# Performance work log

Measured on AMD Instinct MI355X. Metric: run time of the kernel, lower is better.

The kernel has to match this reference:

```python
import jax, jax.numpy as jnp
import numpy as np
from jax import lax

B_, L_ = 2, 512
D_MODEL, EXPAND, HEAD_DIM, NGROUPS, D_STATE, D_CONV = 512, 2, 64, 1, 64, 3
D_INNER = EXPAND * D_MODEL            # 1024
NHEADS = D_INNER // HEAD_DIM          # 16
CONV_DIM = D_INNER + 2 * NGROUPS * D_STATE   # 1152
D_IN_PROJ = 2 * D_INNER + 2 * NGROUPS * D_STATE + NHEADS  # 2192
RMS_EPS = 1e-5


def silu(x):
    return x * jax.nn.sigmoid(x)


def segsum(x):
    # x: (..., T) -> (..., T, T); out[..., i, j] = sum_{j<k<=i} x[..., k], -inf above diag
    T = x.shape[-1]
    xr = jnp.broadcast_to(x[..., None], x.shape + (T,))
    keep = jnp.tril(jnp.ones((T, T), dtype=bool), -1)
    xr = jnp.where(keep, xr, 0.0)
    s = jnp.cumsum(xr, axis=-2)
    diag = jnp.tril(jnp.ones((T, T), dtype=bool), 0)
    return jnp.where(diag, s, -jnp.inf)


def ssd(x, A, Bm, Cm, chunk):
    # x: (b,l,h,p), A: (b,l,h), Bm/Cm: (b,l,g,n); chunk==1 as in the source forward
    b, l, h, p = x.shape
    c = l // chunk
    n = Bm.shape[-1]
    x = x.reshape(b, c, chunk, h, p)
    Bm = Bm.reshape(b, c, chunk, Bm.shape[2], n)
    Cm = Cm.reshape(b, c, chunk, Cm.shape[2], n)
    A = A.reshape(b, c, chunk, h).transpose(0, 3, 1, 2)        # (b,h,c,l)
    A_cumsum = jnp.cumsum(A, axis=-1)
    Lmat = jnp.exp(segsum(A))                                   # (b,h,c,l,l)
    # broadcast group dim (g==1) to heads, matching torch.einsum broadcasting
    Bb = jnp.broadcast_to(Bm, (b, c, chunk, h, n))
    Cb = jnp.broadcast_to(Cm, (b, c, chunk, h, n))
    Y_diag = jnp.einsum('bclhn,bcshn,bhcls,bcshp->bclhp', Cb, Bb, Lmat, x)
    decay_states = jnp.exp(A_cumsum[:, :, :, -1:] - A_cumsum)   # (b,h,c,l)
    states = jnp.einsum('bclhn,bhcl,bclhp->bchpn', Bb, decay_states, x)
    states = jnp.concatenate([jnp.zeros_like(states[:, :1]), states], axis=1)  # (b,c+1,h,p,n)
    A_last = jnp.pad(A_cumsum[:, :, :, -1], ((0, 0), (0, 0), (1, 0)))          # (b,h,c+1)
    decay_chunk = jnp.exp(segsum(A_last))                       # (b,h,c+1,c+1)
    new_states = jnp.einsum('bhzc,bchpn->bzhpn', decay_chunk, states)
    states = new_states[:, :-1]                                 # (b,c,h,p,n)
    state_decay_out = jnp.exp(A_cumsum)
    Y_off = jnp.einsum('bclhn,bchpn,bhcl->bclhp', Cb, states, state_decay_out)
    return (Y_diag + Y_off).reshape(b, l, h, p)


def causal_dwconv(x, w, bias):
    # x: (B,L,C); w: (C,K) depthwise; torch pads (K-1) both sides then slices [:L] == left-pad only
    xt = x.transpose(0, 2, 1)
    y = lax.conv_general_dilated(xt, w[:, None, :], (1,), [(D_CONV - 1, 0)],
                                 feature_group_count=CONV_DIM,
                                 dimension_numbers=('NCH', 'OIH', 'NCH'))
    return y.transpose(0, 2, 1) + bias


def setup_inputs() -> dict:
    key = jax.random.key(0)
    ks = jax.random.split(key, 8)
    u = jax.random.normal(ks[0], (B_, L_, D_MODEL), dtype=jnp.float32)
    W_in = jax.random.normal(ks[1], (D_MODEL, D_IN_PROJ), dtype=jnp.float32) / np.sqrt(D_MODEL).astype(np.float32)
    conv_w = jax.random.normal(ks[2], (CONV_DIM, D_CONV), dtype=jnp.float32) * 0.3
    conv_b = jnp.zeros((CONV_DIM,), dtype=jnp.float32)
    dt = jnp.exp(jax.random.uniform(ks[3], (NHEADS,), dtype=jnp.float32)
                 * (np.float32(np.log(0.1)) - np.float32(np.log(0.001))) + np.float32(np.log(0.001)))
    dt = jnp.clip(dt, 1e-4, None)
    dt_bias = dt + jnp.log(-jnp.expm1(-dt))
    A_log = jnp.log(jax.random.uniform(ks[4], (NHEADS,), dtype=jnp.float32, minval=1.0, maxval=16.0))
    D_param = jnp.ones((NHEADS,), dtype=jnp.float32)
    rms_w = jnp.ones((D_INNER,), dtype=jnp.float32)
    W_out = jax.random.normal(ks[5], (D_INNER, D_MODEL), dtype=jnp.float32) / np.sqrt(D_INNER).astype(np.float32)
    return {"u": u, "W_in": W_in, "conv_w": conv_w, "conv_b": conv_b, "dt_bias": dt_bias,
            "A_log": A_log, "D_param": D_param, "rms_w": rms_w, "W_out": W_out}


def reference(u, W_in, conv_w, conv_b, dt_bias, A_log, D_param, rms_w, W_out):
    b, l, _ = u.shape
    zxbcdt = u @ W_in                                   # (b,l,D_IN_PROJ)
    z = zxbcdt[..., :D_INNER]
    xBC = zxbcdt[..., D_INNER:D_INNER + CONV_DIM]
    dt = zxbcdt[..., D_INNER + CONV_DIM:]
    dt = jax.nn.softplus(dt + dt_bias)                  # (b,l,h)
    A = -jnp.exp(A_log)                                 # (h,)
    xBC = silu(causal_dwconv(xBC, conv_w, conv_b))      # (b,l,CONV_DIM)
    x = xBC[..., :D_INNER].reshape(b, l, NHEADS, HEAD_DIM)
    Bm = xBC[..., D_INNER:D_INNER + D_STATE][:, :, None, :]     # (b,l,1,n)
    Cm = xBC[..., D_INNER + D_STATE:][:, :, None, :]            # (b,l,1,n)
    y = ssd(x * dt[..., None], A * dt, Bm, Cm, 1)       # (b,l,h,p)
    y = y + x * D_param[:, None]
    y = y.reshape(b, l, D_INNER)
    # gated RMSNorm
    yz = y * silu(z)
    y = yz * lax.rsqrt(jnp.mean(yz * yz, axis=-1, keepdims=True) + RMS_EPS) * rms_w
    return y @ W_out
```

## Files before the change

### kernel.cpp

```cpp
#include <hip/hip_runtime.h>
#include <hip/hip_bf16.h>

#define B_SZ 2
#define L_SZ 512
#define D_MODEL 512
#define D_INNER 1024
#define HEAD_DIM 64
#define NHEADS 16
#define D_STATE 64
#define D_CONV 3
#define CONV_DIM 1152
#define D_IN_PROJ 2192
#define BL (B_SZ * L_SZ)
#define RMS_EPS 1e-5f
#define QC 64
#define NCH 8
#define NPAD1 2304
#define PB 72

typedef __attribute__((ext_vector_type(8))) short short8t;
typedef __attribute__((ext_vector_type(8))) unsigned short ushort8t;
typedef __attribute__((ext_vector_type(4))) unsigned short ushort4t;
typedef __attribute__((ext_vector_type(4))) float f32x4;

__device__ __forceinline__ unsigned short f2bf(float f) {
    unsigned u = __float_as_uint(f);
    u += 0x7fff + ((u >> 16) & 1);
    return (unsigned short)(u >> 16);
}
__device__ __forceinline__ float bf2f(unsigned short u) {
    return __uint_as_float(((unsigned)u) << 16);
}

__device__ __forceinline__ void gload_lds16(const void* g, void* lds) {
    __builtin_amdgcn_global_load_lds(
        (const __attribute__((address_space(1))) unsigned int*)g,
        (__attribute__((address_space(3))) unsigned int*)lds, 16, 0, 0);
}

__device__ __forceinline__ void transpose_tile_bf16(const float* __restrict__ src,
                                                    unsigned short* __restrict__ dst,
                                                    int K, int Nin, int tile, int ntn) {
    __shared__ float T[64][65];
    int tid = threadIdx.x;
    int nt = tile % ntn, kt = tile / ntn;
    int n0 = nt * 64, k0 = kt * 64;
#pragma unroll
    for (int rr = 0; rr < 4; ++rr) {
        int k = k0 + (tid >> 4) + rr * 16;
        int nn = (tid & 15) * 4;
#pragma unroll
        for (int q = 0; q < 4; ++q) {
            int n = n0 + nn + q;
            T[(tid >> 4) + rr * 16][nn + q] = (n < Nin) ? src[(size_t)k * Nin + n] : 0.f;
        }
    }
    __syncthreads();
    int nn2 = tid >> 2, kc = tid & 3;
    unsigned short ov[16];
#pragma unroll
    for (int j = 0; j < 16; ++j) ov[j] = f2bf(T[kc * 16 + j][nn2]);
    unsigned short* p = dst + (size_t)(n0 + nn2) * K + k0 + kc * 16;
    *(ushort8t*)p = *(ushort8t*)&ov[0];
    *(ushort8t*)(p + 8) = *(ushort8t*)&ov[8];
}

__global__ __launch_bounds__(256) void prep_kernel(const float* __restrict__ W_in,
                                                   const float* __restrict__ W_out,
                                                   const float* __restrict__ u,
                                                   unsigned short* __restrict__ Wt1,
                                                   unsigned short* __restrict__ Wt2,
                                                   unsigned short* __restrict__ u_bf) {
    int bid = blockIdx.x;
    if (bid < 288) {
        transpose_tile_bf16(W_in, Wt1, D_MODEL, D_IN_PROJ, bid, 36);
    } else if (bid < 416) {
        transpose_tile_bf16(W_out, Wt2, D_INNER, D_MODEL, bid - 288, 8);
    } else {
        int i = ((bid - 416) * 256 + threadIdx.x) * 8;
        float4 v0 = *(const float4*)(u + i);
        float4 v1 = *(const float4*)(u + i + 4);
        unsigned short ov[8] = {f2bf(v0.x), f2bf(v0.y), f2bf(v0.z), f2bf(v0.w),
                                f2bf(v1.x), f2bf(v1.y), f2bf(v1.z), f2bf(v1.w)};
        *(ushort8t*)(u_bf + i) = *(ushort8t*)&ov[0];
    }
}

__global__ __launch_bounds__(256) void gemm_mfma64(const unsigned short* __restrict__ A,
                                                   const unsigned short* __restrict__ Bt,
                                                   float* __restrict__ C,
                                                   int N, int K) {
    __shared__ char sm[49152];
    int tid = threadIdx.x;
    int w = tid >> 6, l = tid & 63;
    int m0 = blockIdx.y * 64, n0 = blockIdx.x * 64;
    int wm = w >> 1, wn = w & 1;

    f32x4 acc[2][2];
#pragma unroll
    for (int i = 0; i < 2; ++i)
#pragma unroll
        for (int j = 0; j < 2; ++j) acc[i][j] = (f32x4){0.f, 0.f, 0.f, 0.f};

    auto stage = [&](const unsigned short* src, int row0, int k0, char* dst) {
#pragma unroll
        for (int p = 0; p < 2; ++p) {
            int c = w * 2 + p;
            int row = c * 8 + (l >> 3);
            int scb = ((l & 7) << 4) ^ ((row & 7) << 4);
            gload_lds16(src + (size_t)(row0 + row) * K + k0 + (scb >> 1), dst + c * 1024);
        }
    };

    int nkt = K / 64;
    stage(A, m0, 0, sm);
    stage(Bt, n0, 0, sm + 8192);
    if (nkt > 1) {
        stage(A, m0, 64, sm + 16384);
        stage(Bt, n0, 64, sm + 16384 + 8192);
    }

    for (int kt = 0; kt < nkt; ++kt) {
        if (kt + 2 < nkt) {
            char* d = sm + ((kt + 2) % 3) * 16384;
            stage(A, m0, (kt + 2) * 64, d);
            stage(Bt, n0, (kt + 2) * 64, d + 8192);
        }
        int inflight = nkt - 1 - kt;
        if (inflight >= 2)      asm volatile("s_waitcnt vmcnt(8)" ::: "memory");
        else if (inflight == 1) asm volatile("s_waitcnt vmcnt(4)" ::: "memory");
        else                    asm volatile("s_waitcnt vmcnt(0)" ::: "memory");
        __builtin_amdgcn_s_barrier();

        const char* Ab = sm + (kt % 3) * 16384;
        const char* Bb = Ab + 8192;
#pragma unroll
        for (int kk = 0; kk < 2; ++kk) {
            short8t af[2], bf[2];
#pragma unroll
            for (int i = 0; i < 2; ++i) {
                int r = wm * 32 + i * 16 + (l & 15);
                int cb = (kk * 64 + (l >> 4) * 16) ^ ((r & 7) << 4);
                af[i] = *(const short8t*)(Ab + r * 128 + cb);
            }
#pragma unroll
            for (int j = 0; j < 2; ++j) {
                int r = wn * 32 + j * 16 + (l & 15);
                int cb = (kk * 64 + (l >> 4) * 16) ^ ((r & 7) << 4);
                bf[j] = *(const short8t*)(Bb + r * 128 + cb);
            }
#pragma unroll
            for (int i = 0; i < 2; ++i)
#pragma unroll
                for (int j = 0; j < 2; ++j)
                    acc[i][j] = __builtin_amdgcn_mfma_f32_16x16x32_bf16(af[i], bf[j], acc[i][j], 0, 0, 0);
        }
        __builtin_amdgcn_s_barrier();
    }

#pragma unroll
    for (int i = 0; i < 2; ++i)
#pragma unroll
        for (int j = 0; j < 2; ++j) {
            int row = m0 + wm * 32 + i * 16 + (l >> 4) * 4;
            int col = n0 + wn * 32 + j * 16 + (l & 15);
            if (col < N) {
#pragma unroll
                for (int r = 0; r < 4; ++r)
                    C[(size_t)(row + r) * N + col] = acc[i][j][r];
            }
        }
}

__global__ __launch_bounds__(256) void gemm_mfma32(const unsigned short* __restrict__ A,
                                                   const unsigned short* __restrict__ Bt,
                                                   float* __restrict__ C,
                                                   int N, int K) {
    __shared__ char sm[36864];
    int tid = threadIdx.x;
    int w = tid >> 6, l = tid & 63;
    int m0 = blockIdx.y * 32, n0 = blockIdx.x * 64;
    int wm = w >> 1, wn = w & 1;

    f32x4 acc[2];
    acc[0] = (f32x4){0.f, 0.f, 0.f, 0.f};
    acc[1] = (f32x4){0.f, 0.f, 0.f, 0.f};

    auto stageA = [&](int k0, char* dst) {
        int row = w * 8 + (l >> 3);
        int scb = ((l & 7) << 4) ^ ((row & 7) << 4);
        gload_lds16(A + (size_t)(m0 + row) * K + k0 + (scb >> 1), dst + w * 1024);
    };
    auto stageB = [&](int k0, char* dst) {
#pragma unroll
        for (int p = 0; p < 2; ++p) {
            int c = w * 2 + p;
            int row = c * 8 + (l >> 3);
            int scb = ((l & 7) << 4) ^ ((row & 7) << 4);
            gload_lds16(Bt + (size_t)(n0 + row) * K + k0 + (scb >> 1), dst + c * 1024);
        }
    };

    int nkt = K / 64;
    stageA(0, sm); stageB(0, sm + 4096);
    stageA(64, sm + 12288); stageB(64, sm + 12288 + 4096);

    for (int kt = 0; kt < nkt; ++kt) {
        if (kt + 2 < nkt) {
            char* d = sm + ((kt + 2) % 3) * 12288;
            stageA((kt + 2) * 64, d);
            stageB((kt + 2) * 64, d + 4096);
        }
        int inflight = nkt - 1 - kt;
        if (inflight >= 2)      asm volatile("s_waitcnt vmcnt(6)" ::: "memory");
        else if (inflight == 1) asm volatile("s_waitcnt vmcnt(3)" ::: "memory");
        else                    asm volatile("s_waitcnt vmcnt(0)" ::: "memory");
        __builtin_amdgcn_s_barrier();

        const char* Ab = sm + (kt % 3) * 12288;
        const char* Bb = Ab + 4096;
#pragma unroll
        for (int kk = 0; kk < 2; ++kk) {
            short8t af;
            {
                int r = wm * 16 + (l & 15);
                int cb = (kk * 64 + (l >> 4) * 16) ^ ((r & 7) << 4);
                af = *(const short8t*)(Ab + r * 128 + cb);
            }
#pragma unroll
            for (int j = 0; j < 2; ++j) {
                int r = wn * 32 + j * 16 + (l & 15);
                int cb = (kk * 64 + (l >> 4) * 16) ^ ((r & 7) << 4);
                short8t bfv = *(const short8t*)(Bb + r * 128 + cb);
                acc[j] = __builtin_amdgcn_mfma_f32_16x16x32_bf16(af, bfv, acc[j], 0, 0, 0);
            }
        }
        __builtin_amdgcn_s_barrier();
    }

#pragma unroll
    for (int j = 0; j < 2; ++j) {
        int col = n0 + wn * 32 + j * 16 + (l & 15);
        int rowb = m0 + wm * 16 + (l >> 4) * 4;
#pragma unroll
        for (int r = 0; r < 4; ++r)
            C[(size_t)(rowb + r) * N + col] = acc[j][r];
    }
}

__device__ __forceinline__ float4 conv4(const float* __restrict__ prow, int gl, int zxcol,
                                        const float* __restrict__ conv_w,
                                        const float* __restrict__ conv_b) {
    float4 v2 = *(const float4*)(prow + zxcol);
    float4 v1 = make_float4(0.f, 0.f, 0.f, 0.f), v0 = v1;
    if (gl >= 1) v1 = *(const float4*)(prow - D_IN_PROJ + zxcol);
    if (gl >= 2) v0 = *(const float4*)(prow - 2 * D_IN_PROJ + zxcol);
    int ch = zxcol - D_INNER;
    float4 o;
    float a;
    a = conv_b[ch+0] + conv_w[(ch+0)*3]*v0.x + conv_w[(ch+0)*3+1]*v1.x + conv_w[(ch+0)*3+2]*v2.x;
    o.x = a / (1.f + __expf(-a));
    a = conv_b[ch+1] + conv_w[(ch+1)*3]*v0.y + conv_w[(ch+1)*3+1]*v1.y + conv_w[(ch+1)*3+2]*v2.y;
    o.y = a / (1.f + __expf(-a));
    a = conv_b[ch+2] + conv_w[(ch+2)*3]*v0.z + conv_w[(ch+2)*3+1]*v1.z + conv_w[(ch+2)*3+2]*v2.z;
    o.z = a / (1.f + __expf(-a));
    a = conv_b[ch+3] + conv_w[(ch+3)*3]*v0.w + conv_w[(ch+3)*3+1]*v1.w + conv_w[(ch+3)*3+2]*v2.w;
    o.w = a / (1.f + __expf(-a));
    return o;
}

__global__ __launch_bounds__(256) void ssd_passA(const float* __restrict__ zxbcdt,
                                                 const float* __restrict__ conv_w,
                                                 const float* __restrict__ conv_b,
                                                 const float* __restrict__ dt_bias,
                                                 const float* __restrict__ A_log,
                                                 const float* __restrict__ D_param,
                                                 float* __restrict__ y,
                                                 float* __restrict__ Zbuf,
                                                 float* __restrict__ Ebuf) {
    int blk = blockIdx.x;
    int h = blk & 15;
    int c = (blk >> 4) & 7;
    int b = blk >> 7;
    int tid = threadIdx.x;

    __shared__ __align__(16) unsigned short Cs_bf[QC][PB];
    __shared__ __align__(16) unsigned short Bs_bf[QC][PB];
    __shared__ __align__(16) unsigned short XDT_bf[QC][PB];
    __shared__ __align__(16) unsigned short BTw_bf[QC][PB];
    __shared__ float csh[QC], dts[QC], wh[QC];
#define PS_bf Cs_bf

    int bl0 = b * L_SZ + c * QC;
    const float* zb = zxbcdt + (size_t)bl0 * D_IN_PROJ;

    if (tid < 64) {
        int t = tid;
        float draw = zb[(size_t)t * D_IN_PROJ + 2 * D_INNER + 2 * D_STATE + h];
        float dtv = draw + dt_bias[h];
        dtv = (dtv > 20.f) ? dtv : log1pf(expf(dtv));
        float A = -expf(A_log[h]);
        float cs = A * dtv;
#pragma unroll
        for (int off = 1; off < 64; off <<= 1) {
            float tmp = __shfl_up(cs, off);
            if (t >= off) cs += tmp;
        }
        float cs63 = __shfl(cs, 63);
        dts[t] = dtv;
        csh[t] = cs;
        wh[t] = __expf(cs63 - cs);
        Ebuf[(((size_t)(b * NHEADS + h) * NCH) + c) * QC + t] = __expf(cs);
    }

    int row16 = tid >> 4;
    int col4 = (tid & 15) * 4;
#pragma unroll
    for (int r = 0; r < 4; ++r) {
        int t = r * 16 + row16;
        int gl = c * QC + t;
        const float* prow = zb + (size_t)t * D_IN_PROJ;
        float4 Bv = conv4(prow, gl, D_INNER + D_INNER + col4, conv_w, conv_b);
        float4 Cv = conv4(prow, gl, D_INNER + D_INNER + D_STATE + col4, conv_w, conv_b);
        ushort4t bq = {f2bf(Bv.x), f2bf(Bv.y), f2bf(Bv.z), f2bf(Bv.w)};
        ushort4t cq = {f2bf(Cv.x), f2bf(Cv.y), f2bf(Cv.z), f2bf(Cv.w)};
        *(ushort4t*)&Bs_bf[t][col4] = bq;
        *(ushort4t*)&Cs_bf[t][col4] = cq;
    }
    __syncthreads();

#pragma unroll
    for (int r = 0; r < 4; ++r) {
        int t = r * 16 + row16;
        int gl = c * QC + t;
        const float* prow = zb + (size_t)t * D_IN_PROJ;
        float4 xv = conv4(prow, gl, D_INNER + h * HEAD_DIM + col4, conv_w, conv_b);
        float d = dts[t], wt = wh[t];
        xv.x *= d; xv.y *= d; xv.z *= d; xv.w *= d;
        ushort4t xq = {f2bf(xv.x), f2bf(xv.y), f2bf(xv.z), f2bf(xv.w)};
        ushort4t bq = *(ushort4t*)&Bs_bf[t][col4];
#pragma unroll
        for (int q = 0; q < 4; ++q) {
            XDT_bf[col4 + q][t] = xq[q];
            BTw_bf[col4 + q][t] = f2bf(bf2f(bq[q]) * wt);
        }
    }
    __syncthreads();

    int l = tid & 63, wv = tid >> 6;
    int wm = wv >> 1, wn = wv & 1;
    int fr = l & 15, fq = l >> 4;

    f32x4 g[2][2];
    {
#pragma unroll
        for (int i = 0; i < 2; ++i)
#pragma unroll
            for (int j = 0; j < 2; ++j) g[i][j] = (f32x4){0.f, 0.f, 0.f, 0.f};
#pragma unroll
        for (int kk = 0; kk < 2; ++kk) {
            short8t af[2], bb[2];
#pragma unroll
            for (int i = 0; i < 2; ++i)
                af[i] = *(const short8t*)&Cs_bf[wm * 32 + i * 16 + fr][kk * 32 + fq * 8];
#pragma unroll
            for (int j = 0; j < 2; ++j)
                bb[j] = *(const short8t*)&Bs_bf[wn * 32 + j * 16 + fr][kk * 32 + fq * 8];
#pragma unroll
            for (int i = 0; i < 2; ++i)
#pragma unroll
                for (int j = 0; j < 2; ++j)
                    g[i][j] = __builtin_amdgcn_mfma_f32_16x16x32_bf16(af[i], bb[j], g[i][j], 0, 0, 0);
        }
    }
    __syncthreads();

    {
#pragma unroll
        for (int i = 0; i < 2; ++i)
#pragma unroll
            for (int j = 0; j < 2; ++j) {
                int s = wn * 32 + j * 16 + fr;
                float css = csh[s];
#pragma unroll
                for (int r = 0; r < 4; ++r) {
                    int t = wm * 32 + i * 16 + fq * 4 + r;
                    float v = (s <= t) ? g[i][j][r] * __expf(csh[t] - css) : 0.f;
                    PS_bf[t][s] = f2bf(v);
                }
            }
    }
    __syncthreads();

    {
        f32x4 yv[2][2];
#pragma unroll
        for (int i = 0; i < 2; ++i)
#pragma unroll
            for (int j = 0; j < 2; ++j) yv[i][j] = (f32x4){0.f, 0.f, 0.f, 0.f};
#pragma unroll
        for (int kk = 0; kk < 2; ++kk) {
            short8t af[2], bb[2];
#pragma unroll
            for (int i = 0; i < 2; ++i)
                af[i] = *(const short8t*)&PS_bf[wm * 32 + i * 16 + fr][kk * 32 + fq * 8];
#pragma unroll
            for (int j = 0; j < 2; ++j)
                bb[j] = *(const short8t*)&XDT_bf[wn * 32 + j * 16 + fr][kk * 32 + fq * 8];
#pragma unroll
            for (int i = 0; i < 2; ++i)
#pragma unroll
                for (int j = 0; j < 2; ++j)
                    yv[i][j] = __builtin_amdgcn_mfma_f32_16x16x32_bf16(af[i], bb[j], yv[i][j], 0, 0, 0);
        }
        float Dp = D_param[h];
#pragma unroll
        for (int i = 0; i < 2; ++i)
#pragma unroll
            for (int j = 0; j < 2; ++j) {
                int p = wn * 32 + j * 16 + fr;
#pragma unroll
                for (int r = 0; r < 4; ++r) {
                    int t = wm * 32 + i * 16 + fq * 4 + r;
                    float xval = bf2f(XDT_bf[p][t]);
                    float fct = Dp / dts[t];
                    y[(size_t)(bl0 + t) * D_INNER + h * HEAD_DIM + p] =
                        yv[i][j][r] + fct * xval;
                }
            }
    }

    {
        f32x4 zv[2][2];
#pragma unroll
        for (int i = 0; i < 2; ++i)
#pragma unroll
            for (int j = 0; j < 2; ++j) zv[i][j] = (f32x4){0.f, 0.f, 0.f, 0.f};
#pragma unroll
        for (int kk = 0; kk < 2; ++kk) {
            short8t af[2], bb[2];
#pragma unroll
            for (int i = 0; i < 2; ++i)
                af[i] = *(const short8t*)&XDT_bf[wm * 32 + i * 16 + fr][kk * 32 + fq * 8];
#pragma unroll
            for (int j = 0; j < 2; ++j)
                bb[j] = *(const short8t*)&BTw_bf[wn * 32 + j * 16 + fr][kk * 32 + fq * 8];
#pragma unroll
            for (int i = 0; i < 2; ++i)
#pragma unroll
                for (int j = 0; j < 2; ++j)
                    zv[i][j] = __builtin_amdgcn_mfma_f32_16x16x32_bf16(af[i], bb[j], zv[i][j], 0, 0, 0);
        }
        float* Zr = Zbuf + (((size_t)(b * NHEADS + h) * NCH) + c) * (HEAD_DIM * D_STATE);
#pragma unroll
        for (int i = 0; i < 2; ++i)
#pragma unroll
            for (int j = 0; j < 2; ++j) {
                int n = wn * 32 + j * 16 + fr;
#pragma unroll
                for (int r = 0; r < 4; ++r) {
                    int p = wm * 32 + i * 16 + fq * 4 + r;
                    Zr[p * D_STATE + n] = zv[i][j][r];
                }
            }
    }
#undef PS_bf
}

__global__ __launch_bounds__(256) void ssd_passC(const float* __restrict__ zxbcdt,
                                                 const float* __restrict__ conv_w,
                                                 const float* __restrict__ conv_b,
                                                 const float* __restrict__ Zbuf,
                                                 const float* __restrict__ Ebuf,
                                                 float* __restrict__ y) {
    int blk = blockIdx.x;
    int h = blk & 15;
    int q = blk >> 4;
    int c = 1 + (q % 7);
    int b = q / 7;
    int tid = threadIdx.x;

    __shared__ __align__(16) unsigned short Cs_bf[QC][PB];
    __shared__ __align__(16) unsigned short S_bf[QC][PB];
    __shared__ float Eh[QC];

    int bl0 = b * L_SZ + c * QC;
    const float* zb = zxbcdt + (size_t)bl0 * D_IN_PROJ;
    const float* Zb = Zbuf + ((size_t)(b * NHEADS + h) * NCH) * (HEAD_DIM * D_STATE);
    const float* Eb = Ebuf + ((size_t)(b * NHEADS + h) * NCH) * QC;

    {
        int p = tid >> 2, nq = (tid & 3) * 16;
        float S16[16];
#pragma unroll
        for (int qq = 0; qq < 16; ++qq) S16[qq] = 0.f;
        float wgt = 1.f;
        for (int j = c - 1; j >= 0; --j) {
            const float* Zj = Zb + (size_t)j * (HEAD_DIM * D_STATE) + p * D_STATE + nq;
#pragma unroll
            for (int q4 = 0; q4 < 4; ++q4) {
                float4 z = *(const float4*)(Zj + q4 * 4);
                S16[q4 * 4 + 0] += wgt * z.x;
                S16[q4 * 4 + 1] += wgt * z.y;
                S16[q4 * 4 + 2] += wgt * z.z;
                S16[q4 * 4 + 3] += wgt * z.w;
            }
            wgt *= Eb[(size_t)j * QC + 63];
        }
#pragma unroll
        for (int q4 = 0; q4 < 4; ++q4) {
            ushort4t s4 = {f2bf(S16[q4 * 4 + 0]), f2bf(S16[q4 * 4 + 1]),
                           f2bf(S16[q4 * 4 + 2]), f2bf(S16[q4 * 4 + 3])};
            *(ushort4t*)&S_bf[p][nq + q4 * 4] = s4;
        }
    }

    int row16 = tid >> 4, col4 = (tid & 15) * 4;
#pragma unroll
    for (int r = 0; r < 4; ++r) {
        int t = r * 16 + row16;
        int gl = c * QC + t;
        float4 Cv = conv4(zb + (size_t)t * D_IN_PROJ, gl,
                          D_INNER + D_INNER + D_STATE + col4, conv_w, conv_b);
        ushort4t cq = {f2bf(Cv.x), f2bf(Cv.y), f2bf(Cv.z), f2bf(Cv.w)};
        *(ushort4t*)&Cs_bf[t][col4] = cq;
    }
    if (tid < 64)
        Eh[tid] = Ebuf[(((size_t)(b * NHEADS + h) * NCH) + c) * QC + tid];
    __syncthreads();

    int l = tid & 63, wv = tid >> 6;
    int wm = wv >> 1, wn = wv & 1;
    int fr = l & 15, fq = l >> 4;
    f32x4 acc[2][2];
#pragma unroll
    for (int i = 0; i < 2; ++i)
#pragma unroll
        for (int j = 0; j < 2; ++j) acc[i][j] = (f32x4){0.f, 0.f, 0.f, 0.f};
#pragma unroll
    for (int kk = 0; kk < 2; ++kk) {
        short8t af[2], bb[2];
#pragma unroll
        for (int i = 0; i < 2; ++i)
            af[i] = *(const short8t*)&Cs_bf[wm * 32 + i * 16 + fr][kk * 32 + fq * 8];
#pragma unroll
        for (int j = 0; j < 2; ++j)
            bb[j] = *(const short8t*)&S_bf[wn * 32 + j * 16 + fr][kk * 32 + fq * 8];
#pragma unroll
        for (int i = 0; i < 2; ++i)
#pragma unroll
            for (int j = 0; j < 2; ++j)
                acc[i][j] = __builtin_amdgcn_mfma_f32_16x16x32_bf16(af[i], bb[j], acc[i][j], 0, 0, 0);
    }
#pragma unroll
    for (int i = 0; i < 2; ++i)
#pragma unroll
        for (int j = 0; j < 2; ++j) {
            int p = wn * 32 + j * 16 + fr;
#pragma unroll
            for (int r = 0; r < 4; ++r) {
                int t = wm * 32 + i * 16 + fq * 4 + r;
                float* yp = y + (size_t)(bl0 + t) * D_INNER + h * HEAD_DIM + p;
                *yp += Eh[t] * acc[i][j][r];
            }
        }
}

__global__ __launch_bounds__(256) void gated_rmsnorm_kernel(const float* __restrict__ zxbcdt,
                                                            const float* __restrict__ y,
                                                            const float* __restrict__ rms_w,
                                                            unsigned short* __restrict__ yn_bf) {
    int bl = blockIdx.x;
    int tid = threadIdx.x;
    __shared__ float red[4];
    __shared__ float sscale;
    float vals[4];
    float sumsq = 0.f;
#pragma unroll
    for (int i = 0; i < 4; ++i) {
        int col = tid + i * 256;
        float yv = y[(size_t)bl * D_INNER + col];
        float z = zxbcdt[(size_t)bl * D_IN_PROJ + col];
        float yz = yv * (z / (1.f + expf(-z)));
        vals[i] = yz;
        sumsq += yz * yz;
    }
#pragma unroll
    for (int off = 32; off; off >>= 1) sumsq += __shfl_xor(sumsq, off);
    int wave = tid >> 6, lane = tid & 63;
    if (lane == 0) red[wave] = sumsq;
    __syncthreads();
    if (tid == 0) {
        float t = red[0] + red[1] + red[2] + red[3];
        sscale = rsqrtf(t / (float)D_INNER + RMS_EPS);
    }
    __syncthreads();
    float sc = sscale;
#pragma unroll
    for (int i = 0; i < 4; ++i) {
        int col = tid + i * 256;
        yn_bf[(size_t)bl * D_INNER + col] = f2bf(vals[i] * sc * rms_w[col]);
    }
}

extern "C" void kernel_launch(void* const* d_in, const int* in_sizes, int n_in,
                              void* d_out, int out_size, void* d_ws, size_t ws_size,
                              hipStream_t stream) {
    const float* u       = (const float*)d_in[0];
    const float* W_in    = (const float*)d_in[1];
    const float* conv_w  = (const float*)d_in[2];
    const float* conv_b  = (const float*)d_in[3];
    const float* dt_bias = (const float*)d_in[4];
    const float* A_log   = (const float*)d_in[5];
    const float* D_param = (const float*)d_in[6];
    const float* rms_w   = (const float*)d_in[7];
    const float* W_out   = (const float*)d_in[8];
    float* out = (float*)d_out;

    float* ws = (float*)d_ws;
    float* zxbcdt = ws;
    float* y      = zxbcdt + (size_t)BL * D_IN_PROJ;
    float* Zbuf   = y + (size_t)BL * D_INNER;
    float* Ebuf   = Zbuf + (size_t)32 * NCH * 4096;
    unsigned short* u_bf  = (unsigned short*)(Ebuf + 32 * NCH * QC);
    unsigned short* Wt1   = u_bf + (size_t)BL * D_MODEL;
    unsigned short* Wt2   = Wt1 + (size_t)NPAD1 * D_MODEL;
    unsigned short* yn_bf = Wt2 + (size_t)D_MODEL * D_INNER;

    prep_kernel<<<672, 256, 0, stream>>>(W_in, W_out, u, Wt1, Wt2, u_bf);

    gemm_mfma64<<<dim3(NPAD1 / 64, BL / 64), 256, 0, stream>>>(
        u_bf, Wt1, zxbcdt, D_IN_PROJ, D_MODEL);

    ssd_passA<<<B_SZ * NCH * NHEADS, 256, 0, stream>>>(
        zxbcdt, conv_w, conv_b, dt_bias, A_log, D_param, y, Zbuf, Ebuf);
    ssd_passC<<<224, 256, 0, stream>>>(
        zxbcdt, conv_w, conv_b, Zbuf, Ebuf, y);

    gated_rmsnorm_kernel<<<BL, 256, 0, stream>>>(zxbcdt, y, rms_w, yn_bf);

    gemm_mfma32<<<dim3(D_MODEL / 64, BL / 32), 256, 0, stream>>>(
        yn_bf, Wt2, out, D_MODEL, D_INNER);
}
```

Measured before the change: 47.67 us.

## Fuse SSD passes, RMSNorm and output GEMM into one persistent kernel with grid barriers

Replaces four separate launches (SSD pass A, pass C, gated RMSNorm, output GEMM) with a single 256-block kernel that runs each stage in turn, separated by atomic-counter grid barriers. The counters are reset inside the prep kernel. The aim is to remove three kernel launch gaps and tail effects. In exchange, RMSNorm now does four rows per block instead of one block per row, and the spin barriers rely on all 256 blocks being co-resident.

```diff
diff --git a/kernel.cpp b/kernel.cpp
--- a/kernel.cpp
+++ b/kernel.cpp
@@ -17,6 +17,7 @@
 #define NCH 8
 #define NPAD1 2304
 #define PB 72
+#define NBLK 256u
 
 typedef __attribute__((ext_vector_type(8))) short short8t;
 typedef __attribute__((ext_vector_type(8))) unsigned short ushort8t;
@@ -36,6 +37,16 @@
     __builtin_amdgcn_global_load_lds(
         (const __attribute__((address_space(1))) unsigned int*)g,
         (__attribute__((address_space(3))) unsigned int*)lds, 16, 0, 0);
+}
+
+__device__ __forceinline__ void grid_barrier(unsigned* cnt, int k) {
+    __syncthreads();
+    if (threadIdx.x == 0) {
+        __hip_atomic_fetch_add(&cnt[k], 1u, __ATOMIC_RELEASE, __HIP_MEMORY_SCOPE_AGENT);
+        while (__hip_atomic_load(&cnt[k], __ATOMIC_ACQUIRE, __HIP_MEMORY_SCOPE_AGENT) < NBLK)
+            __builtin_amdgcn_s_sleep(2);
+    }
+    __syncthreads();
 }
 
 __device__ __forceinline__ void transpose_tile_bf16(const float* __restrict__ src,
@@ -70,8 +81,10 @@
                                                    const float* __restrict__ u,
                                                    unsigned short* __restrict__ Wt1,
                                                    unsigned short* __restrict__ Wt2,
-                                                   unsigned short* __restrict__ u_bf) {
+                                                   unsigned short* __restrict__ u_bf,
+                                                   unsigned* __restrict__ cnt) {
     int bid = blockIdx.x;
+    if (bid == 0 && threadIdx.x < 8) cnt[threadIdx.x] = 0u;
     if (bid < 288) {
         transpose_tile_bf16(W_in, Wt1, D_MODEL, D_IN_PROJ, bid, 36);
     } else if (bid < 416) {
@@ -170,82 +183,6 @@
                     C[(size_t)(row + r) * N + col] = acc[i][j][r];
             }
         }
-}
-
-__global__ __launch_bounds__(256) void gemm_mfma32(const unsigned short* __restrict__ A,
-                                                   const unsigned short* __restrict__ Bt,
-                                                   float* __restrict__ C,
-                                                   int N, int K) {
-    __shared__ char sm[36864];
-    int tid = threadIdx.x;
-    int w = tid >> 6, l = tid & 63;
-    int m0 = blockIdx.y * 32, n0 = blockIdx.x * 64;
-    int wm = w >> 1, wn = w & 1;
-
-    f32x4 acc[2];
-    acc[0] = (f32x4){0.f, 0.f, 0.f, 0.f};
-    acc[1] = (f32x4){0.f, 0.f, 0.f, 0.f};
-
-    auto stageA = [&](int k0, char* dst) {
-        int row = w * 8 + (l >> 3);
-        int scb = ((l & 7) << 4) ^ ((row & 7) << 4);
-        gload_lds16(A + (size_t)(m0 + row) * K + k0 + (scb >> 1), dst + w * 1024);
-    };
-    auto stageB = [&](int k0, char* dst) {
-#pragma unroll
-        for (int p = 0; p < 2; ++p) {
-            int c = w * 2 + p;
-            int row = c * 8 + (l >> 3);
-            int scb = ((l & 7) << 4) ^ ((row & 7) << 4);
-            gload_lds16(Bt + (size_t)(n0 + row) * K + k0 + (scb >> 1), dst + c * 1024);
-        }
-    };
-
-    int nkt = K / 64;
-    stageA(0, sm); stageB(0, sm + 4096);
-    stageA(64, sm + 12288); stageB(64, sm + 12288 + 4096);
-
-    for (int kt = 0; kt < nkt; ++kt) {
-        if (kt + 2 < nkt) {
-            char* d = sm + ((kt + 2) % 3) * 12288;
-            stageA((kt + 2) * 64, d);
-            stageB((kt + 2) * 64, d + 4096);
-        }
-        int inflight = nkt - 1 - kt;
-        if (inflight >= 2)      asm volatile("s_waitcnt vmcnt(6)" ::: "memory");
-        else if (inflight == 1) asm volatile("s_waitcnt vmcnt(3)" ::: "memory");
-        else                    asm volatile("s_waitcnt vmcnt(0)" ::: "memory");
-        __builtin_amdgcn_s_barrier();
-
-        const char* Ab = sm + (kt % 3) * 12288;
-        const char* Bb = Ab + 4096;
-#pragma unroll
-        for (int kk = 0; kk < 2; ++kk) {
-            short8t af;
-            {
-                int r = wm * 16 + (l & 15);
-                int cb = (kk * 64 + (l >> 4) * 16) ^ ((r & 7) << 4);
-                af = *(const short8t*)(Ab + r * 128 + cb);
-            }
-#pragma unroll
-            for (int j = 0; j < 2; ++j) {
-                int r = wn * 32 + j * 16 + (l & 15);
-                int cb = (kk * 64 + (l >> 4) * 16) ^ ((r & 7) << 4);
-                short8t bfv = *(const short8t*)(Bb + r * 128 + cb);
-                acc[j] = __builtin_amdgcn_mfma_f32_16x16x32_bf16(af, bfv, acc[j], 0, 0, 0);
-            }
-        }
-        __builtin_amdgcn_s_barrier();
-    }
-
-#pragma unroll
-    for (int j = 0; j < 2; ++j) {
-        int col = n0 + wn * 32 + j * 16 + (l & 15);
-        int rowb = m0 + wm * 16 + (l >> 4) * 4;
-#pragma unroll
-        for (int r = 0; r < 4; ++r)
-            C[(size_t)(rowb + r) * N + col] = acc[j][r];
-    }
 }
 
 __device__ __forceinline__ float4 conv4(const float* __restrict__ prow, int gl, int zxcol,
@@ -269,27 +206,24 @@
     return o;
 }
 
-__global__ __launch_bounds__(256) void ssd_passA(const float* __restrict__ zxbcdt,
-                                                 const float* __restrict__ conv_w,
-                                                 const float* __restrict__ conv_b,
-                                                 const float* __restrict__ dt_bias,
-                                                 const float* __restrict__ A_log,
-                                                 const float* __restrict__ D_param,
-                                                 float* __restrict__ y,
-                                                 float* __restrict__ Zbuf,
-                                                 float* __restrict__ Ebuf) {
-    int blk = blockIdx.x;
+
+__device__ __forceinline__ void passA_body(int blk, int tid, char* smem,
+        const float* __restrict__ zxbcdt, const float* __restrict__ conv_w,
+        const float* __restrict__ conv_b, const float* __restrict__ dt_bias,
+        const float* __restrict__ A_log, const float* __restrict__ D_param,
+        float* __restrict__ y, float* __restrict__ Zbuf, float* __restrict__ Ebuf) {
     int h = blk & 15;
     int c = (blk >> 4) & 7;
     int b = blk >> 7;
-    int tid = threadIdx.x;
-
-    __shared__ __align__(16) unsigned short Cs_bf[QC][PB];
-    __shared__ __align__(16) unsigned short Bs_bf[QC][PB];
-    __shared__ __align__(16) unsigned short XDT_bf[QC][PB];
-    __shared__ __align__(16) unsigned short BTw_bf[QC][PB];
-    __shared__ float csh[QC], dts[QC], wh[QC];
-#define PS_bf Cs_bf
+
+    unsigned short* Cs  = (unsigned short*)smem;
+    unsigned short* Bs  = Cs + 64 * PB;
+    unsigned short* XDT = Bs + 64 * PB;
+    unsigned short* BTw = XDT + 64 * PB;
+    float* csh = (float*)(smem + 4 * 64 * PB * 2);
+    float* dts = csh + 64;
+    float* wh  = dts + 64;
+#define PS Cs
 
     int bl0 = b * L_SZ + c * QC;
     const float* zb = zxbcdt + (size_t)bl0 * D_IN_PROJ;
@@ -324,8 +258,8 @@
         float4 Cv = conv4(prow, gl, D_INNER + D_INNER + D_STATE + col4, conv_w, conv_b);
         ushort4t bq = {f2bf(Bv.x), f2bf(Bv.y), f2bf(Bv.z), f2bf(Bv.w)};
         ushort4t cq = {f2bf(Cv.x), f2bf(Cv.y), f2bf(Cv.z), f2bf(Cv.w)};
-        *(ushort4t*)&Bs_bf[t][col4] = bq;
-        *(ushort4t*)&Cs_bf[t][col4] = cq;
+        *(ushort4t*)&Bs[t * PB + col4] = bq;
+        *(ushort4t*)&Cs[t * PB + col4] = cq;
     }
     __syncthreads();
 
@@ -338,11 +272,11 @@
         float d = dts[t], wt = wh[t];
         xv.x *= d; xv.y *= d; xv.z *= d; xv.w *= d;
         ushort4t xq = {f2bf(xv.x), f2bf(xv.y), f2bf(xv.z), f2bf(xv.w)};
-        ushort4t bq = *(ushort4t*)&Bs_bf[t][col4];
+        ushort4t bq = *(ushort4t*)&Bs[t * PB + col4];
 #pragma unroll
         for (int q = 0; q < 4; ++q) {
-            XDT_bf[col4 + q][t] = xq[q];
-            BTw_bf[col4 + q][t] = f2bf(bf2f(bq[q]) * wt);
+            XDT[(col4 + q) * PB + t] = xq[q];
+            BTw[(col4 + q) * PB + t] = f2bf(bf2f(bq[q]) * wt);
         }
     }
     __syncthreads();
@@ -362,10 +296,10 @@
             short8t af[2], bb[2];
 #pragma unroll
             for (int i = 0; i < 2; ++i)
-                af[i] = *(const short8t*)&Cs_bf[wm * 32 + i * 16 + fr][kk * 32 + fq * 8];
+                af[i] = *(const short8t*)&Cs[(wm * 32 + i * 16 + fr) * PB + kk * 32 + fq * 8];
 #pragma unroll
             for (int j = 0; j < 2; ++j)
-                bb[j] = *(const short8t*)&Bs_bf[wn * 32 + j * 16 + fr][kk * 32 + fq * 8];
+                bb[j] = *(const short8t*)&Bs[(wn * 32 + j * 16 + fr) * PB + kk * 32 + fq * 8];
 #pragma unroll
             for (int i = 0; i < 2; ++i)
 #pragma unroll
@@ -386,7 +320,7 @@
                 for (int r = 0; r < 4; ++r) {
                     int t = wm * 32 + i * 16 + fq * 4 + r;
                     float v = (s <= t) ? g[i][j][r] * __expf(csh[t] - css) : 0.f;
-                    PS_bf[t][s] = f2bf(v);
+                    PS[t * PB + s] = f2bf(v);
                 }
             }
     }
@@ -403,10 +337,10 @@
             short8t af[2], bb[2];
 #pragma unroll
             for (int i = 0; i < 2; ++i)
-                af[i] = *(const short8t*)&PS_bf[wm * 32 + i * 16 + fr][kk * 32 + fq * 8];
+                af[i] = *(const short8t*)&PS[(wm * 32 + i * 16 + fr) * PB + kk * 32 + fq * 8];
 #pragma unroll
             for (int j = 0; j < 2; ++j)
-                bb[j] = *(const short8t*)&XDT_bf[wn * 32 + j * 16 + fr][kk * 32 + fq * 8];
+                bb[j] = *(const short8t*)&XDT[(wn * 32 + j * 16 + fr) * PB + kk * 32 + fq * 8];
 #pragma unroll
             for (int i = 0; i < 2; ++i)
 #pragma unroll
@@ -422,7 +356,7 @@
 #pragma unroll
                 for (int r = 0; r < 4; ++r) {
                     int t = wm * 32 + i * 16 + fq * 4 + r;
-                    float xval = bf2f(XDT_bf[p][t]);
+                    float xval = bf2f(XDT[p * PB + t]);
                     float fct = Dp / dts[t];
                     y[(size_t)(bl0 + t) * D_INNER + h * HEAD_DIM + p] =
                         yv[i][j][r] + fct * xval;
@@ -441,10 +375,10 @@
             short8t af[2], bb[2];
 #pragma unroll
             for (int i = 0; i < 2; ++i)
-                af[i] = *(const short8t*)&XDT_bf[wm * 32 + i * 16 + fr][kk * 32 + fq * 8];
+                af[i] = *(const short8t*)&XDT[(wm * 32 + i * 16 + fr) * PB + kk * 32 + fq * 8];
 #pragma unroll
             for (int j = 0; j < 2; ++j)
-                bb[j] = *(const short8t*)&BTw_bf[wn * 32 + j * 16 + fr][kk * 32 + fq * 8];
+                bb[j] = *(const short8t*)&BTw[(wn * 32 + j * 16 + fr) * PB + kk * 32 + fq * 8];
 #pragma unroll
             for (int i = 0; i < 2; ++i)
 #pragma unroll
@@ -464,25 +398,21 @@
                 }
             }
     }
-#undef PS_bf
-}
-
-__global__ __launch_bounds__(256) void ssd_passC(const float* __restrict__ zxbcdt,
-                                                 const float* __restrict__ conv_w,
-                                                 const float* __restrict__ conv_b,
-                                                 const float* __restrict__ Zbuf,
-                                                 const float* __restrict__ Ebuf,
-                                                 float* __restrict__ y) {
-    int blk = blockIdx.x;
+#undef PS
+}
+
+__device__ __forceinline__ void passC_body(int blk, int tid, char* smem,
+        const float* __restrict__ zxbcdt, const float* __restrict__ conv_w,
+        const float* __restrict__ conv_b, const float* __restrict__ Zbuf,
+        const float* __restrict__ Ebuf, float* __restrict__ y) {
     int h = blk & 15;
     int q = blk >> 4;
     int c = 1 + (q % 7);
     int b = q / 7;
-    int tid = threadIdx.x;
-
-    __shared__ __align__(16) unsigned short Cs_bf[QC][PB];
-    __shared__ __align__(16) unsigned short S_bf[QC][PB];
-    __shared__ float Eh[QC];
+
+    unsigned short* Cs = (unsigned short*)smem;
+    unsigned short* S  = Cs + 64 * PB;
+    float* Eh = (float*)(smem + 2 * 64 * PB * 2);
 
     int bl0 = b * L_SZ + c * QC;
     const float* zb = zxbcdt + (size_t)bl0 * D_IN_PROJ;
@@ -511,7 +441,7 @@
         for (int q4 = 0; q4 < 4; ++q4) {
             ushort4t s4 = {f2bf(S16[q4 * 4 + 0]), f2bf(S16[q4 * 4 + 1]),
                            f2bf(S16[q4 * 4 + 2]), f2bf(S16[q4 * 4 + 3])};
-            *(ushort4t*)&S_bf[p][nq + q4 * 4] = s4;
+            *(ushort4t*)&S[p * PB + nq + q4 * 4] = s4;
         }
     }
 
@@ -523,7 +453,7 @@
         float4 Cv = conv4(zb + (size_t)t * D_IN_PROJ, gl,
                           D_INNER + D_INNER + D_STATE + col4, conv_w, conv_b);
         ushort4t cq = {f2bf(Cv.x), f2bf(Cv.y), f2bf(Cv.z), f2bf(Cv.w)};
-        *(ushort4t*)&Cs_bf[t][col4] = cq;
+        *(ushort4t*)&Cs[t * PB + col4] = cq;
     }
     if (tid < 64)
         Eh[tid] = Ebuf[(((size_t)(b * NHEADS + h) * NCH) + c) * QC + tid];
@@ -542,10 +472,10 @@
         short8t af[2], bb[2];
 #pragma unroll
         for (int i = 0; i < 2; ++i)
-            af[i] = *(const short8t*)&Cs_bf[wm * 32 + i * 16 + fr][kk * 32 + fq * 8];
+            af[i] = *(const short8t*)&Cs[(wm * 32 + i * 16 + fr) * PB + kk * 32 + fq * 8];
 #pragma unroll
         for (int j = 0; j < 2; ++j)
-            bb[j] = *(const short8t*)&S_bf[wn * 32 + j * 16 + fr][kk * 32 + fq * 8];
+            bb[j] = *(const short8t*)&S[(wn * 32 + j * 16 + fr) * PB + kk * 32 + fq * 8];
 #pragma unroll
         for (int i = 0; i < 2; ++i)
 #pragma unroll
@@ -566,41 +496,147 @@
         }
 }
 
-__global__ __launch_bounds__(256) void gated_rmsnorm_kernel(const float* __restrict__ zxbcdt,
-                                                            const float* __restrict__ y,
-                                                            const float* __restrict__ rms_w,
-                                                            unsigned short* __restrict__ yn_bf) {
-    int bl = blockIdx.x;
-    int tid = threadIdx.x;
-    __shared__ float red[4];
-    __shared__ float sscale;
-    float vals[4];
-    float sumsq = 0.f;
-#pragma unroll
-    for (int i = 0; i < 4; ++i) {
-        int col = tid + i * 256;
-        float yv = y[(size_t)bl * D_INNER + col];
-        float z = zxbcdt[(size_t)bl * D_IN_PROJ + col];
-        float yz = yv * (z / (1.f + expf(-z)));
-        vals[i] = yz;
-        sumsq += yz * yz;
-    }
-#pragma unroll
-    for (int off = 32; off; off >>= 1) sumsq += __shfl_xor(sumsq, off);
-    int wave = tid >> 6, lane = tid & 63;
-    if (lane == 0) red[wave] = sumsq;
-    __syncthreads();
-    if (tid == 0) {
-        float t = red[0] + red[1] + red[2] + red[3];
-        sscale = rsqrtf(t / (float)D_INNER + RMS_EPS);
-    }
-    __syncthreads();
-    float sc = sscale;
-#pragma unroll
-    for (int i = 0; i < 4; ++i) {
-        int col = tid + i * 256;
-        yn_bf[(size_t)bl * D_INNER + col] = f2bf(vals[i] * sc * rms_w[col]);
-    }
+__device__ __forceinline__ void norm_body(int blk, int tid, char* smem,
+        const float* __restrict__ zxbcdt, const float* __restrict__ y,
+        const float* __restrict__ rms_w, unsigned short* __restrict__ yn_bf) {
+    float* red = (float*)smem;
+    float* ssc = red + 4;
+    for (int rr = 0; rr < 4; ++rr) {
+        int bl = blk * 4 + rr;
+        float vals[4];
+        float sumsq = 0.f;
+#pragma unroll
+        for (int i = 0; i < 4; ++i) {
+            int col = tid + i * 256;
+            float yv = y[(size_t)bl * D_INNER + col];
+            float z = zxbcdt[(size_t)bl * D_IN_PROJ + col];
+            float yz = yv * (z / (1.f + __expf(-z)));
+            vals[i] = yz;
+            sumsq += yz * yz;
+        }
+#pragma unroll
+        for (int off = 32; off; off >>= 1) sumsq += __shfl_xor(sumsq, off);
+        int wave = tid >> 6, lane = tid & 63;
+        if (lane == 0) red[wave] = sumsq;
+        __syncthreads();
+        if (tid == 0) {
+            float t = red[0] + red[1] + red[2] + red[3];
+            ssc[0] = rsqrtf(t / (float)D_INNER + RMS_EPS);
+        }
+        __syncthreads();
+        float sc = ssc[0];
+#pragma unroll
+        for (int i = 0; i < 4; ++i) {
+            int col = tid + i * 256;
+            yn_bf[(size_t)bl * D_INNER + col] = f2bf(vals[i] * sc * rms_w[col]);
+        }
+        __syncthreads();
+    }
+}
+
+__device__ __forceinline__ void gemm2_body(int blk, int tid, char* smem,
+        const unsigned short* __restrict__ A, const unsigned short* __restrict__ Bt,
+        float* __restrict__ out) {
+    const int K = D_INNER, N = D_MODEL;
+    int w = tid >> 6, l = tid & 63;
+    int n0 = (blk & 7) * 64, m0 = (blk >> 3) * 32;
+    int wm = w >> 1, wn = w & 1;
+
+    f32x4 acc[2];
+    acc[0] = (f32x4){0.f, 0.f, 0.f, 0.f};
+    acc[1] = (f32x4){0.f, 0.f, 0.f, 0.f};
+
+    auto stageA = [&](int k0, char* dst) {
+        int row = w * 8 + (l >> 3);
+        int scb = ((l & 7) << 4) ^ ((row & 7) << 4);
+        gload_lds16(A + (size_t)(m0 + row) * K + k0 + (scb >> 1), dst + w * 1024);
+    };
+    auto stageB = [&](int k0, char* dst) {
+#pragma unroll
+        for (int p = 0; p < 2; ++p) {
+            int c = w * 2 + p;
+            int row = c * 8 + (l >> 3);
+            int scb = ((l & 7) << 4) ^ ((row & 7) << 4);
+            gload_lds16(Bt + (size_t)(n0 + row) * K + k0 + (scb >> 1), dst + c * 1024);
+        }
+    };
+
+    const int nkt = K / 64;
+    stageA(0, smem); stageB(0, smem + 4096);
+    stageA(64, smem + 12288); stageB(64, smem + 12288 + 4096);
+
+    for (int kt = 0; kt < nkt; ++kt) {
+        if (kt + 2 < nkt) {
+            char* d = smem + ((kt + 2) % 3) * 12288;
+            stageA((kt + 2) * 64, d);
+            stageB((kt + 2) * 64, d + 4096);
+        }
+        int inflight = nkt - 1 - kt;
+        if (inflight >= 2)      asm volatile("s_waitcnt vmcnt(6)" ::: "memory");
+        else if (inflight == 1) asm volatile("s_waitcnt vmcnt(3)" ::: "memory");
+        else                    asm volatile("s_waitcnt vmcnt(0)" ::: "memory");
+        __builtin_amdgcn_s_barrier();
+
+        const char* Ab = smem + (kt % 3) * 12288;
+        const char* Bb = Ab + 4096;
+#pragma unroll
+        for (int kk = 0; kk < 2; ++kk) {
+            short8t af;
+            {
+                int r = wm * 16 + (l & 15);
+                int cb = (kk * 64 + (l >> 4) * 16) ^ ((r & 7) << 4);
+                af = *(const short8t*)(Ab + r * 128 + cb);
+            }
+#pragma unroll
+            for (int j = 0; j < 2; ++j) {
+                int r = wn * 32 + j * 16 + (l & 15);
+                int cb = (kk * 64 + (l >> 4) * 16) ^ ((r & 7) << 4);
+                short8t bfv = *(const short8t*)(Bb + r * 128 + cb);
+                acc[j] = __builtin_amdgcn_mfma_f32_16x16x32_bf16(af, bfv, acc[j], 0, 0, 0);
+            }
+        }
+        __builtin_amdgcn_s_barrier();
+    }
+
+#pragma unroll
+    for (int j = 0; j < 2; ++j) {
+        int col = n0 + wn * 32 + j * 16 + (l & 15);
+        int rowb = m0 + wm * 16 + (l >> 4) * 4;
+#pragma unroll
+        for (int r = 0; r < 4; ++r)
+            out[(size_t)(rowb + r) * N + col] = acc[j][r];
+    }
+}
+
+__global__ __launch_bounds__(256) void ssd_mega(const float* __restrict__ zxbcdt,
+                                                const float* __restrict__ conv_w,
+                                                const float* __restrict__ conv_b,
+                                                const float* __restrict__ dt_bias,
+                                                const float* __restrict__ A_log,
+                                                const float* __restrict__ D_param,
+                                                const float* __restrict__ rms_w,
+                                                const unsigned short* __restrict__ Wt2,
+                                                float* __restrict__ y,
+                                                float* __restrict__ Zbuf,
+                                                float* __restrict__ Ebuf,
+                                                unsigned short* __restrict__ yn_bf,
+                                                float* __restrict__ out,
+                                                unsigned* __restrict__ cnt) {
+    __shared__ __align__(16) char smem[37632];
+    int blk = blockIdx.x, tid = threadIdx.x;
+
+    passA_body(blk, tid, smem, zxbcdt, conv_w, conv_b, dt_bias, A_log, D_param,
+               y, Zbuf, Ebuf);
+    grid_barrier(cnt, 0);
+
+    if (blk < 224)
+        passC_body(blk, tid, smem, zxbcdt, conv_w, conv_b, Zbuf, Ebuf, y);
+    grid_barrier(cnt, 1);
+
+    norm_body(blk, tid, smem, zxbcdt, y, rms_w, yn_bf);
+    grid_barrier(cnt, 2);
+
+    gemm2_body(blk, tid, smem, yn_bf, Wt2, out);
 }
 
 extern "C" void kernel_launch(void* const* d_in, const int* in_sizes, int n_in,
@@ -626,19 +662,14 @@
     unsigned short* Wt1   = u_bf + (size_t)BL * D_MODEL;
     unsigned short* Wt2   = Wt1 + (size_t)NPAD1 * D_MODEL;
     unsigned short* yn_bf = Wt2 + (size_t)D_MODEL * D_INNER;
-
-    prep_kernel<<<672, 256, 0, stream>>>(W_in, W_out, u, Wt1, Wt2, u_bf);
+    unsigned* cnt = (unsigned*)(yn_bf + (size_t)BL * D_INNER);
+
+    prep_kernel<<<672, 256, 0, stream>>>(W_in, W_out, u, Wt1, Wt2, u_bf, cnt);
 
     gemm_mfma64<<<dim3(NPAD1 / 64, BL / 64), 256, 0, stream>>>(
         u_bf, Wt1, zxbcdt, D_IN_PROJ, D_MODEL);
 
-    ssd_passA<<<B_SZ * NCH * NHEADS, 256, 0, stream>>>(
-        zxbcdt, conv_w, conv_b, dt_bias, A_log, D_param, y, Zbuf, Ebuf);
-    ssd_passC<<<224, 256, 0, stream>>>(
-        zxbcdt, conv_w, conv_b, Zbuf, Ebuf, y);
-
-    gated_rmsnorm_kernel<<<BL, 256, 0, stream>>>(zxbcdt, y, rms_w, yn_bf);
-
-    gemm_mfma32<<<dim3(D_MODEL / 64, BL / 32), 256, 0, stream>>>(
-        yn_bf, Wt2, out, D_MODEL, D_INNER);
-}
+    ssd_mega<<<NBLK, 256, 0, stream>>>(
+        zxbcdt, conv_w, conv_b, dt_bias, A_log, D_param, rms_w, Wt2,
+        y, Zbuf, Ebuf, yn_bf, out, cnt);
+}
```

New measurement: 102.9 us. +115.9%, slower.
